# Performance work log

Measured on AMD Instinct MI355X. Metric: run time of the kernel, lower is better.

## Reference

```python
import jax, jax.numpy as jnp
import numpy as np

B, C, T = 1024, 64, 275
S = 10            # number of subjects
EMB = 184         # encoder embedding dim
PROJ = 1024       # projector dim
LN_EPS = 1e-5


def setup_inputs() -> dict:
    key = jax.random.key(0)
    ks = jax.random.split(key, 12)
    sc = lambda *shape: 1.0 / np.sqrt(shape[-1] if len(shape) > 1 else 1.0)
    return {
        "eeg": jax.random.normal(ks[0], (B, C, T), dtype=jnp.float32),
        "subject_ids": jax.random.randint(ks[1], (B,), 0, S, dtype=jnp.int64),
        # per-subject Linear(T, T): y = x @ W.T + b
        "subj_W": jax.random.normal(ks[2], (S, T, T), dtype=jnp.float32) / np.sqrt(T),
        "subj_b": jax.random.normal(ks[3], (S, T), dtype=jnp.float32) * 0.02,
        # encoder stub: flatten (C*T) -> Linear -> EMB
        "enc_W": jax.random.normal(ks[4], (C * T, EMB), dtype=jnp.float32) / np.sqrt(C * T),
        "enc_b": jnp.zeros((EMB,), dtype=jnp.float32),
        # projector: Linear(EMB, PROJ) -> ResidualAdd(GELU -> Linear(PROJ, PROJ)) -> LayerNorm
        "W1": jax.random.normal(ks[5], (EMB, PROJ), dtype=jnp.float32) / np.sqrt(EMB),
        "b1": jnp.zeros((PROJ,), dtype=jnp.float32),
        "W2": jax.random.normal(ks[6], (PROJ, PROJ), dtype=jnp.float32) / np.sqrt(PROJ),
        "b2": jnp.zeros((PROJ,), dtype=jnp.float32),
        "gamma": jnp.ones((PROJ,), dtype=jnp.float32),
        "beta": jnp.zeros((PROJ,), dtype=jnp.float32),
    }


def reference(eeg, subject_ids, subj_W, subj_b, enc_W, enc_b, W1, b1, W2, b2, gamma, beta):
    # --- subject-wise alignment: grouped gather -> linear -> scatter ---
    # Vectorized form of the per-subject loop: each row b uses weight subj_W[sid[b]].
    Wg = subj_W[subject_ids]              # [B, T, T]
    bg = subj_b[subject_ids]              # [B, T]
    # torch Linear: y = x @ W.T + b  ->  y[b,c,u] = sum_t eeg[b,c,t] * Wg[b,u,t]
    x = jnp.einsum("bct,but->bcu", eeg, Wg) + bg[:, None, :]   # [B, C, T]

    # --- encoder stub (SpatioTemporalCNN placeholder): flatten + linear ---
    h = x.reshape(x.shape[0], -1) @ enc_W + enc_b              # [B, EMB]

    # --- MLPProjector ---
    h = h @ W1 + b1                                            # [B, PROJ]
    r = jax.nn.gelu(h, approximate=False) @ W2 + b2            # dropout is identity at eval
    h = h + r
    # LayerNorm over last dim
    mu = jnp.mean(h, axis=-1, keepdims=True)
    var = jnp.mean(jnp.square(h - mu), axis=-1, keepdims=True)
    out = (h - mu) * jax.lax.rsqrt(var + LN_EPS) * gamma + beta
    return out
```

## Files before the change

### kernel.cpp

```cpp
#include <hip/hip_runtime.h>
#include <math.h>

#define B_N    1024
#define C_N    64
#define T_N    275
#define S_N    10
#define EMB_N  184
#define PROJ_N 1024
#define CT_N   (C_N * T_N)
#define TP     288
#define KP2    (TP * C_N)
#define EMBP   192
#define KZ2    32
#define KC2    (KP2 / KZ2)
#define KZ5    2
#define GMAX   264

typedef unsigned short u16;
typedef __attribute__((ext_vector_type(8))) short short8;
typedef __attribute__((ext_vector_type(4))) short short4v;
typedef __attribute__((ext_vector_type(4))) float f32x4;

#define MFMA16(a,b,c) __builtin_amdgcn_mfma_f32_16x16x32_bf16(a, b, c, 0, 0, 0)

__device__ __forceinline__ u16 f2bf(float f) {
    union { float f; unsigned u; } v; v.f = f;
    unsigned r = v.u + 0x7FFFu + ((v.u >> 16) & 1u);
    return (u16)(r >> 16);
}
__device__ __forceinline__ float gelu_exact(float v) {
    return 0.5f * v * (1.0f + erff(v * 0.70710678118654752f));
}
__device__ __forceinline__ void gload16(const void* g, void* lds) {
    __builtin_amdgcn_global_load_lds(
        (const __attribute__((address_space(1))) void*)g,
        (__attribute__((address_space(3))) void*)lds, 16, 0, 0);
}

__global__ __launch_bounds__(256) void p_all(
    const float* __restrict__ eeg, const int* __restrict__ sid,
    const float* __restrict__ W, const float* __restrict__ encW,
    const float* __restrict__ W1, const float* __restrict__ W2,
    u16* __restrict__ eegb, u16* __restrict__ Wb, u16* __restrict__ eT,
    u16* __restrict__ w1t, u16* __restrict__ w2t, int* __restrict__ bsq)
{
    __shared__ char smem[16640];
    const int blk = blockIdx.x;
    const int tid = threadIdx.x;

    if (blk < 1024) {
        const int b = blk;
        const float* src = eeg + (size_t)b * CT_N;
        u16* dst = eegb + (size_t)b * C_N * TP;
        #pragma unroll
        for (int p = 0; p < 9; ++p) {
            int ch = tid + p * 256;
            int c = ch / 36, q8 = ch - c * 36;
            int t0 = q8 * 8;
            short8 pk;
            #pragma unroll
            for (int e = 0; e < 8; ++e) {
                int t = t0 + e;
                float v = (t < T_N) ? src[c * T_N + t] : 0.f;
                pk[e] = (short)f2bf(v);
            }
            *reinterpret_cast<short8*>(dst + c * TP + t0) = pk;
        }
        return;
    }
    if (blk < 1834) {
        int idx4 = (blk - 1024) * 256 + tid;
        if (idx4 >= S_N * TP * TP / 4) return;
        int o = idx4 * 4;
        int row = o / TP, t = o - row * TP;
        int s = row / TP, u = row - s * TP;
        short4v pk;
        #pragma unroll
        for (int e = 0; e < 4; ++e) {
            float v = (u < T_N && t + e < T_N)
                ? W[((size_t)s * T_N + u) * T_N + t + e] : 0.f;
            pk[e] = (short)f2bf(v);
        }
        *reinterpret_cast<short4v*>(Wb + o) = pk;
        return;
    }
    if (blk < 2698) {
        float (*tile)[65] = (float(*)[65])smem;
        int local = blk - 1834;
        const int t = local / 3;
        const int n0 = (local % 3) * 64;
        const int j = tid & 63, cg = tid >> 6;
        #pragma unroll
        for (int pass = 0; pass < 16; ++pass) {
            int c = pass * 4 + cg;
            float v = 0.f;
            if (t < T_N && n0 + j < EMB_N)
                v = encW[((size_t)c * T_N + t) * EMB_N + n0 + j];
            tile[c][j] = v;
        }
        __syncthreads();
        #pragma unroll
        for (int pass = 0; pass < 16; ++pass) {
            int nl = pass * 4 + cg;
            eT[(size_t)(n0 + nl) * KP2 + t * 64 + j] = f2bf(tile[j][nl]);
        }
        return;
    }
    if (blk < 2746) {
        float (*tile)[65] = (float(*)[65])smem;
        int local = blk - 2698;
        const int k0 = (local % 3) * 64, n0 = (local / 3) * 64;
        for (int l = tid; l < 4096; l += 256) {
            int i = l >> 6, j = l & 63;
            float v = (k0 + i < EMB_N) ? W1[(size_t)(k0 + i) * PROJ_N + n0 + j] : 0.f;
            tile[i][j] = v;
        }
        __syncthreads();
        for (int l = tid; l < 4096; l += 256) {
            int j = l >> 6, i = l & 63;
            w1t[(size_t)(n0 + j) * EMBP + k0 + i] = f2bf(tile[i][j]);
        }
        return;
    }
    if (blk < 3002) {
        float (*tile)[65] = (float(*)[65])smem;
        int local = blk - 2746;
        const int k0 = (local % 16) * 64, n0 = (local / 16) * 64;
        for (int l = tid; l < 4096; l += 256) {
            int i = l >> 6, j = l & 63;
            tile[i][j] = W2[(size_t)(k0 + i) * PROJ_N + n0 + j];
        }
        __syncthreads();
        for (int l = tid; l < 4096; l += 256) {
            int j = l >> 6, i = l & 63;
            w2t[(size_t)(n0 + j) * PROJ_N + k0 + i] = f2bf(tile[i][j]);
        }
        return;
    }
    {
        int* sgrp = (int*)smem;
        int* C    = (int*)(smem + 4096);
        int* tot  = (int*)(smem + 4096 + 640);
        for (int i = tid; i < 1024; i += 256) sgrp[i] = sid[i];
        for (int i = tid; i < 4 * GMAX; i += 256) bsq[i] = -1;
        __syncthreads();
        const int w4 = tid >> 6, lane = tid & 63;
        #pragma unroll
        for (int j = 0; j < 4; ++j) {
            int chunk = w4 * 4 + j;
            int sb = sgrp[chunk * 64 + lane];
            int myc = 0;
            for (int s = 0; s < S_N; ++s) {
                unsigned long long m = __ballot(sb == s);
                if (lane == s) myc = (int)__popcll(m);
            }
            if (lane < S_N) C[chunk * S_N + lane] = myc;
        }
        __syncthreads();
        if (tid < S_N) {
            int a = 0;
            for (int w2 = 0; w2 < 16; ++w2) a += C[w2 * S_N + tid];
            tot[tid] = a;
        }
        __syncthreads();
        #pragma unroll
        for (int rep = 0; rep < 4; ++rep) {
            int b = tid + rep * 256;
            int s = sgrp[b];
            int off = 0;
            for (int s2 = 0; s2 < S_N; ++s2)
                if (s2 < s) off += (tot[s2] + 3) & ~3;
            int chunk = b >> 6;
            int rank = 0;
            for (int w2 = 0; w2 < 16; ++w2)
                if (w2 < chunk) rank += C[w2 * S_N + s];
            for (int i = chunk * 64; i < b; ++i) rank += (sgrp[i] == s) ? 1 : 0;
            bsq[off + rank] = b;
        }
    }
}

__global__ __launch_bounds__(512, 2) void k1g(
    const u16* __restrict__ eegb, const int* __restrict__ sid,
    const u16* __restrict__ Wb, const float* __restrict__ subj_b,
    const int* __restrict__ bsq, u16* __restrict__ xb)
{
    __shared__ u16 Bs[2][TP * 4 * 8];
    const int g = blockIdx.x;
    const int b0 = bsq[g * 4];
    if (b0 < 0) return;
    const int s = sid[b0];
    const int tid = threadIdx.x;
    const int w = tid >> 6, lane = tid & 63;
    const int bi = w >> 1, uh = w & 1;
    const int lrow = lane & 15, lk = lane >> 4;
    const int b = bsq[g * 4 + bi];
    const int bsafe = (b >= 0) ? b : 0;
    const u16* A = eegb + (size_t)bsafe * C_N * TP;
    const u16* Wr = Wb + (size_t)s * TP * TP;

    #define K1_STAGE(st, ks)                                                   \
        for (int l = tid; l < TP * 4; l += 512) {                              \
            int u_ = l >> 2, q_ = l & 3;                                       \
            gload16(Wr + (size_t)u_ * TP + (ks) * 32 + ((q_ ^ ((u_ >> 1) & 3)) << 3), \
                    &Bs[st][l * 8]);                                           \
        }

    f32x4 acc[4][9] = {};
    short8 a[4], an[4];

    K1_STAGE(0, 0);
    #pragma unroll
    for (int rt = 0; rt < 4; ++rt)
        a[rt] = *reinterpret_cast<const short8*>(A + (16 * rt + lrow) * TP + 8 * lk);
    __syncthreads();

    for (int ks = 0; ks < 9; ++ks) {
        const int st = ks & 1;
        if (ks < 8) {
            K1_STAGE(st ^ 1, ks + 1);
            #pragma unroll
            for (int rt = 0; rt < 4; ++rt)
                an[rt] = *reinterpret_cast<const short8*>(
                    A + (16 * rt + lrow) * TP + (ks + 1) * 32 + 8 * lk);
        }
        #pragma unroll
        for (int ct = 0; ct < 9; ++ct) {
            int u = uh * 144 + 16 * ct + lrow;
            int chunk = u * 4 + (lk ^ ((u >> 1) & 3));
            short8 bv = *reinterpret_cast<const short8*>(&Bs[st][chunk * 8]);
            #pragma unroll
            for (int rt = 0; rt < 4; ++rt)
                acc[rt][ct] = MFMA16(a[rt], bv, acc[rt][ct]);
        }
        __syncthreads();
        #pragma unroll
        for (int rt = 0; rt < 4; ++rt) a[rt] = an[rt];
    }

    if (b < 0) return;
    #pragma unroll
    for (int ct = 0; ct < 9; ++ct) {
        int u = uh * 144 + 16 * ct + lrow;
        if (u >= T_N) continue;
        float bias = subj_b[s * T_N + u];
        #pragma unroll
        for (int rt = 0; rt < 4; ++rt) {
            int c0 = 16 * rt + 4 * lk;
            short4v pk;
            #pragma unroll
            for (int r = 0; r < 4; ++r)
                pk[r] = (short)f2bf(acc[rt][ct][r] + bias);
            *reinterpret_cast<short4v*>(xb + ((size_t)b * TP + u) * C_N + c0) = pk;
        }
    }
    #undef K1_STAGE
}

__global__ __launch_bounds__(256) void k2_mfma(
    const u16* __restrict__ xb, const u16* __restrict__ eT,
    float* __restrict__ part)
{
    __shared__ u16 Ab[2][128 * 64];
    const int m0 = blockIdx.x * 128;
    const int kz = blockIdx.y;
    const int kbase = kz * KC2;
    const int tid = threadIdx.x;
    const int w = tid >> 6, lane = tid & 63;
    const int lrow = lane & 15, lk = lane >> 4;

    #define K2_STAGE(st, step)                                                 \
        _Pragma("unroll")                                                      \
        for (int p = 0; p < 4; ++p) {                                          \
            int l = tid + p * 256;                                             \
            int r_ = l >> 3, q_ = l & 7;                                       \
            gload16(xb + (size_t)(m0 + r_) * KP2 + kbase + (step) * 64 +       \
                        ((q_ ^ (r_ & 7)) << 3),                                \
                    &Ab[st][l * 8]);                                           \
        }

    #define K2_BLOAD(step, dst)                                                \
        _Pragma("unroll")                                                      \
        for (int ct = 0; ct < 3; ++ct)                                         \
            _Pragma("unroll")                                                  \
            for (int ki = 0; ki < 2; ++ki)                                     \
                dst[ct][ki] = *reinterpret_cast<const short8*>(                \
                    eT + (size_t)(48 * w + 16 * ct + lrow) * KP2 + kbase +     \
                    (step) * 64 + ki * 32 + 8 * lk);

    f32x4 acc[8][3] = {};
    short8 bf[3][2], bn[3][2];

    K2_STAGE(0, 0);
    K2_BLOAD(0, bf);
    __syncthreads();

    for (int step = 0; step < 9; ++step) {
        const int st = step & 1;
        if (step < 8) {
            K2_STAGE(st ^ 1, step + 1);
            K2_BLOAD(step + 1, bn);
        }
        #pragma unroll
        for (int ki = 0; ki < 2; ++ki)
            #pragma unroll
            for (int rt = 0; rt < 8; ++rt) {
                int m = 16 * rt + lrow;
                int chunk = m * 8 + ((4 * ki + lk) ^ (m & 7));
                short8 af = *reinterpret_cast<const short8*>(&Ab[st][chunk * 8]);
                #pragma unroll
                for (int ct = 0; ct < 3; ++ct)
                    acc[rt][ct] = MFMA16(af, bf[ct][ki], acc[rt][ct]);
            }
        __syncthreads();
        #pragma unroll
        for (int ct = 0; ct < 3; ++ct)
            #pragma unroll
            for (int ki = 0; ki < 2; ++ki) bf[ct][ki] = bn[ct][ki];
    }

    #pragma unroll
    for (int rt = 0; rt < 8; ++rt)
        #pragma unroll
        for (int ct = 0; ct < 3; ++ct) {
            int n = 48 * w + 16 * ct + lrow;
            #pragma unroll
            for (int r = 0; r < 4; ++r) {
                int m = m0 + 16 * rt + 4 * lk + r;
                part[((size_t)kz * B_N + m) * EMBP + n] = acc[rt][ct][r];
            }
        }
    #undef K2_STAGE
    #undef K2_BLOAD
}

__global__ __launch_bounds__(256) void k3_reduce(
    const float* __restrict__ part, const float* __restrict__ enc_b,
    u16* __restrict__ hb)
{
    int idx = blockIdx.x * 256 + threadIdx.x;
    if (idx >= B_N * EMBP) return;
    int n = idx % EMBP;
    float s = 0.f;
    if (n < EMB_N) {
        s = enc_b[n];
        #pragma unroll
        for (int z = 0; z < KZ2; ++z)
            s += part[(size_t)z * B_N * EMBP + idx];
    }
    hb[idx] = f2bf(s);
}

__global__ __launch_bounds__(256) void k4_mfma(
    const u16* __restrict__ hb, const u16* __restrict__ w1t,
    const float* __restrict__ b1, float* __restrict__ h1, u16* __restrict__ g)
{
    __shared__ u16 Ab[64 * EMBP];
    __shared__ u16 Bb[64 * EMBP];
    const int m0 = blockIdx.x * 64, n0 = blockIdx.y * 64;
    const int tid = threadIdx.x;
    const int w = tid >> 6, lane = tid & 63;
    const int wr = w >> 1, wc = w & 1;
    const int lrow = lane & 15, lk = lane >> 4;

    #pragma unroll
    for (int i = 0; i < 6; ++i) {
        int L = tid + i * 256;
        int row = L / 24, qp = L % 24;
        int ql = qp ^ (row & 7);
        gload16(hb  + (size_t)(m0 + row) * EMBP + ql * 8, &Ab[(size_t)L * 8]);
        gload16(w1t + (size_t)(n0 + row) * EMBP + ql * 8, &Bb[(size_t)L * 8]);
    }
    __syncthreads();

    f32x4 acc[2][2] = {};
    #pragma unroll
    for (int ks = 0; ks < 6; ++ks) {
        #pragma unroll
        for (int rt = 0; rt < 2; ++rt) {
            int c = 32 * wr + 16 * rt + lrow;
            short8 af = *reinterpret_cast<const short8*>(
                &Ab[c * EMBP + (((4 * ks + lk) ^ (c & 7)) * 8)]);
            #pragma unroll
            for (int ct = 0; ct < 2; ++ct) {
                int nl = 32 * wc + 16 * ct + lrow;
                short8 bfv = *reinterpret_cast<const short8*>(
                    &Bb[nl * EMBP + (((4 * ks + lk) ^ (nl & 7)) * 8)]);
                acc[rt][ct] = MFMA16(af, bfv, acc[rt][ct]);
            }
        }
    }
    #pragma unroll
    for (int rt = 0; rt < 2; ++rt)
        #pragma unroll
        for (int ct = 0; ct < 2; ++ct) {
            int n = n0 + 32 * wc + 16 * ct + lrow;
            #pragma unroll
            for (int r = 0; r < 4; ++r) {
                int m = m0 + 32 * wr + 16 * rt + 4 * lk + r;
                float v = acc[rt][ct][r] + b1[n];
                size_t o = (size_t)m * PROJ_N + n;
                h1[o] = v;
                g[o] = f2bf(gelu_exact(v));
            }
        }
}

__global__ __launch_bounds__(256) void k5_mfma(
    const u16* __restrict__ g, const u16* __restrict__ w2t,
    float* __restrict__ part2)
{
    __shared__ u16 Ab[2][64 * 64];
    __shared__ u16 Bb[2][64 * 64];
    const int m0 = blockIdx.x * 64, n0 = blockIdx.y * 64;
    const int kz = blockIdx.z;
    const int kbase = kz * (PROJ_N / KZ5);
    const int tid = threadIdx.x;
    const int w = tid >> 6, lane = tid & 63;
    const int wr = w >> 1, wc = w & 1;
    const int lrow = lane & 15, lk = lane >> 4;

    const int r0 = tid >> 3, q0 = tid & 7;
    const int r1 = (tid + 256) >> 3;
    const u16* a0 = g + (size_t)(m0 + r0) * PROJ_N + (q0 ^ (r0 & 7)) * 8;
    const u16* a1 = g + (size_t)(m0 + r1) * PROJ_N + (q0 ^ (r1 & 7)) * 8;
    const u16* b0 = w2t + (size_t)(n0 + r0) * PROJ_N + (q0 ^ (r0 & 7)) * 8;
    const u16* b1p = w2t + (size_t)(n0 + r1) * PROJ_N + (q0 ^ (r1 & 7)) * 8;

    f32x4 acc[2][2] = {};
    int buf = 0;
    gload16(a0 + kbase, &Ab[0][(size_t)(w * 64) * 8]);
    gload16(a1 + kbase, &Ab[0][(size_t)(w * 64 + 256) * 8]);
    gload16(b0 + kbase, &Bb[0][(size_t)(w * 64) * 8]);
    gload16(b1p + kbase, &Bb[0][(size_t)(w * 64 + 256) * 8]);
    __syncthreads();

    for (int step = 0; step < 8; ++step) {
        if (step < 7) {
            int k0 = kbase + (step + 1) * 64;
            gload16(a0 + k0, &Ab[buf ^ 1][(size_t)(w * 64) * 8]);
            gload16(a1 + k0, &Ab[buf ^ 1][(size_t)(w * 64 + 256) * 8]);
            gload16(b0 + k0, &Bb[buf ^ 1][(size_t)(w * 64) * 8]);
            gload16(b1p + k0, &Bb[buf ^ 1][(size_t)(w * 64 + 256) * 8]);
        }
        #pragma unroll
        for (int ki = 0; ki < 2; ++ki) {
            #pragma unroll
            for (int rt = 0; rt < 2; ++rt) {
                int c = 32 * wr + 16 * rt + lrow;
                short8 af = *reinterpret_cast<const short8*>(
                    &Ab[buf][c * 64 + (((lk + 4 * ki) ^ (c & 7)) * 8)]);
                #pragma unroll
                for (int ct = 0; ct < 2; ++ct) {
                    int nl = 32 * wc + 16 * ct + lrow;
                    short8 bfv = *reinterpret_cast<const short8*>(
                        &Bb[buf][nl * 64 + (((lk + 4 * ki) ^ (nl & 7)) * 8)]);
                    acc[rt][ct] = MFMA16(af, bfv, acc[rt][ct]);
                }
            }
        }
        __syncthreads();
        buf ^= 1;
    }
    #pragma unroll
    for (int rt = 0; rt < 2; ++rt)
        #pragma unroll
        for (int ct = 0; ct < 2; ++ct) {
            int n = n0 + 32 * wc + 16 * ct + lrow;
            #pragma unroll
            for (int r = 0; r < 4; ++r) {
                int m = m0 + 32 * wr + 16 * rt + 4 * lk + r;
                part2[(size_t)kz * B_N * PROJ_N + (size_t)m * PROJ_N + n] = acc[rt][ct][r];
            }
        }
}

__global__ __launch_bounds__(256) void k5r_ln(
    const float* __restrict__ part2, const float* __restrict__ h1,
    const float* __restrict__ b2, const float* __restrict__ gamma,
    const float* __restrict__ beta, float* __restrict__ out)
{
    const int m = blockIdx.x;
    const int tid = threadIdx.x;
    const float4* h4 = reinterpret_cast<const float4*>(h1 + (size_t)m * PROJ_N);
    const float4* p0 = reinterpret_cast<const float4*>(part2 + (size_t)m * PROJ_N);
    const float4* p1 = reinterpret_cast<const float4*>(part2 + (size_t)(B_N + m) * PROJ_N);
    const float4* b4 = reinterpret_cast<const float4*>(b2);
    float4 va = h4[tid], vb = p0[tid], vc = p1[tid], vd = b4[tid];
    float v[4] = { va.x + vb.x + vc.x + vd.x, va.y + vb.y + vc.y + vd.y,
                   va.z + vb.z + vc.z + vd.z, va.w + vb.w + vc.w + vd.w };
    float s = 0.f, sq = 0.f;
    #pragma unroll
    for (int i = 0; i < 4; ++i) { s += v[i]; sq += v[i] * v[i]; }
    #pragma unroll
    for (int off = 32; off > 0; off >>= 1) {
        s  += __shfl_down(s, off);
        sq += __shfl_down(sq, off);
    }
    __shared__ float ss[4], ssq[4];
    int wid = tid >> 6, lane = tid & 63;
    if (lane == 0) { ss[wid] = s; ssq[wid] = sq; }
    __syncthreads();
    if (tid == 0) {
        float a = 0.f, bsum = 0.f;
        #pragma unroll
        for (int q = 0; q < 4; ++q) { a += ss[q]; bsum += ssq[q]; }
        ss[0] = a; ssq[0] = bsum;
    }
    __syncthreads();
    float mu  = ss[0] * (1.0f / PROJ_N);
    float var = ssq[0] * (1.0f / PROJ_N) - mu * mu;
    float rs  = rsqrtf(var + 1e-5f);
    const float4 g4 = reinterpret_cast<const float4*>(gamma)[tid];
    const float4 be4 = reinterpret_cast<const float4*>(beta)[tid];
    float gg[4] = { g4.x, g4.y, g4.z, g4.w };
    float bb[4] = { be4.x, be4.y, be4.z, be4.w };
    float4 o4;
    float* op = reinterpret_cast<float*>(&o4);
    #pragma unroll
    for (int i = 0; i < 4; ++i) op[i] = (v[i] - mu) * rs * gg[i] + bb[i];
    reinterpret_cast<float4*>(out + (size_t)m * PROJ_N)[tid] = o4;
}

extern "C" void kernel_launch(void* const* d_in, const int* in_sizes, int n_in,
                              void* d_out, int out_size, void* d_ws, size_t ws_size,
                              hipStream_t stream)
{
    const float* eeg    = (const float*)d_in[0];
    const int*   sid    = (const int*)  d_in[1];
    const float* subj_W = (const float*)d_in[2];
    const float* subj_b = (const float*)d_in[3];
    const float* enc_W  = (const float*)d_in[4];
    const float* enc_b  = (const float*)d_in[5];
    const float* W1     = (const float*)d_in[6];
    const float* b1     = (const float*)d_in[7];
    const float* W2     = (const float*)d_in[8];
    const float* b2     = (const float*)d_in[9];
    const float* gamma  = (const float*)d_in[10];
    const float* beta   = (const float*)d_in[11];
    float* out = (float*)d_out;

    char* w = (char*)d_ws;
    u16*   xb    = (u16*)(w);
    u16*   Wb    = (u16*)(w + 37748736);
    u16*   eT    = (u16*)(w + 39407616);
    u16*   w1t   = (u16*)(w + 46485504);
    u16*   w2t   = (u16*)(w + 46878720);
    u16*   hb    = (u16*)(w + 48975872);
    float* h1    = (float*)(w + 49369088);
    u16*   g     = (u16*)(w + 53563392);
    int*   bsq   = (int*)(w + 55660544);
    char*  scr   = w + 55664896;
    u16*   eegb  = (u16*)scr;
    float* part  = (float*)scr;
    float* part2 = (float*)(scr + 25165824);

    p_all<<<dim3(3003), 256, 0, stream>>>(eeg, sid, subj_W, enc_W, W1, W2,
                                          eegb, Wb, eT, w1t, w2t, bsq);
    k1g  <<<dim3(GMAX), 512, 0, stream>>>(eegb, sid, Wb, subj_b, bsq, xb);
    k2_mfma<<<dim3(8, KZ2), 256, 0, stream>>>(xb, eT, part);
    k3_reduce<<<dim3((B_N * EMBP + 255) / 256), 256, 0, stream>>>(part, enc_b, hb);
    k4_mfma<<<dim3(16, 16), 256, 0, stream>>>(hb, w1t, b1, h1, g);
    k5_mfma<<<dim3(16, 16, KZ5), 256, 0, stream>>>(g, w2t, part2);
    k5r_ln <<<dim3(B_N), 256, 0, stream>>>(part2, h1, b2, gamma, beta, out);
}
```

Before: 132.2 us.

## Fuse eeg bf16 conversion into grouped subject GEMM and retile encoder GEMM

Drops the separate eeg-to-bf16 pre-pass: k1g now reads fp32 eeg directly, converts it in registers and stages it through double-buffered LDS, with the MFMA operands swapped so the output is written in channel-major [c][u] layout. The encoder weight transpose and the k2 K-ordering change to match this layout, and subject bias is pre-padded into a small buffer. k2 moves to 64-row tiles with half the split-K factor, giving more M blocks and fewer partials to reduce. This removes a full write and re-read of the bf16 eeg copy, at the cost of more complex staging and register pressure in k1g.

Result: slower. 173.6 us (+31.4%).

```diff
diff --git a/kernel.cpp b/kernel.cpp
--- a/kernel.cpp
+++ b/kernel.cpp
@@ -9,12 +9,19 @@
 #define PROJ_N 1024
 #define CT_N   (C_N * T_N)
 #define TP     288
-#define KP2    (TP * C_N)
+#define KP2    (C_N * TP)
 #define EMBP   192
-#define KZ2    32
+#define KZ2    16
 #define KC2    (KP2 / KZ2)
 #define KZ5    2
 #define GMAX   264
+
+#define SEC_W   0
+#define SEC_E   810
+#define SEC_1   1002
+#define SEC_2   1050
+#define SEC_G   1306
+#define SEC_N   1307
 
 typedef unsigned short u16;
 typedef __attribute__((ext_vector_type(8))) short short8;
@@ -38,38 +45,18 @@
 }
 
 __global__ __launch_bounds__(256) void p_all(
-    const float* __restrict__ eeg, const int* __restrict__ sid,
-    const float* __restrict__ W, const float* __restrict__ encW,
-    const float* __restrict__ W1, const float* __restrict__ W2,
-    u16* __restrict__ eegb, u16* __restrict__ Wb, u16* __restrict__ eT,
-    u16* __restrict__ w1t, u16* __restrict__ w2t, int* __restrict__ bsq)
+    const int* __restrict__ sid, const float* __restrict__ W,
+    const float* __restrict__ encW, const float* __restrict__ W1,
+    const float* __restrict__ W2, const float* __restrict__ subj_b,
+    u16* __restrict__ Wb, u16* __restrict__ eT, u16* __restrict__ w1t,
+    u16* __restrict__ w2t, int* __restrict__ bsq, float* __restrict__ sbp)
 {
     __shared__ char smem[16640];
     const int blk = blockIdx.x;
     const int tid = threadIdx.x;
 
-    if (blk < 1024) {
-        const int b = blk;
-        const float* src = eeg + (size_t)b * CT_N;
-        u16* dst = eegb + (size_t)b * C_N * TP;
-        #pragma unroll
-        for (int p = 0; p < 9; ++p) {
-            int ch = tid + p * 256;
-            int c = ch / 36, q8 = ch - c * 36;
-            int t0 = q8 * 8;
-            short8 pk;
-            #pragma unroll
-            for (int e = 0; e < 8; ++e) {
-                int t = t0 + e;
-                float v = (t < T_N) ? src[c * T_N + t] : 0.f;
-                pk[e] = (short)f2bf(v);
-            }
-            *reinterpret_cast<short8*>(dst + c * TP + t0) = pk;
-        }
-        return;
-    }
-    if (blk < 1834) {
-        int idx4 = (blk - 1024) * 256 + tid;
+    if (blk < SEC_E) {
+        int idx4 = blk * 256 + tid;
         if (idx4 >= S_N * TP * TP / 4) return;
         int o = idx4 * 4;
         int row = o / TP, t = o - row * TP;
@@ -84,31 +71,35 @@
         *reinterpret_cast<short4v*>(Wb + o) = pk;
         return;
     }
-    if (blk < 2698) {
+    if (blk < SEC_1) {
         float (*tile)[65] = (float(*)[65])smem;
-        int local = blk - 1834;
-        const int t = local / 3;
+        int local = blk - SEC_E;
+        const int c = local / 3;
         const int n0 = (local % 3) * 64;
-        const int j = tid & 63, cg = tid >> 6;
-        #pragma unroll
-        for (int pass = 0; pass < 16; ++pass) {
-            int c = pass * 4 + cg;
-            float v = 0.f;
-            if (t < T_N && n0 + j < EMB_N)
-                v = encW[((size_t)c * T_N + t) * EMB_N + n0 + j];
-            tile[c][j] = v;
-        }
-        __syncthreads();
-        #pragma unroll
-        for (int pass = 0; pass < 16; ++pass) {
-            int nl = pass * 4 + cg;
-            eT[(size_t)(n0 + nl) * KP2 + t * 64 + j] = f2bf(tile[j][nl]);
+        for (int u0 = 0; u0 < TP; u0 += 64) {
+            int wlen = (TP - u0 < 64) ? (TP - u0) : 64;
+            __syncthreads();
+            for (int l = tid; l < 4096; l += 256) {
+                int i = l >> 6, j = l & 63;
+                int u = u0 + i, n = n0 + j;
+                float v = 0.f;
+                if (u < T_N && n < EMB_N)
+                    v = encW[((size_t)c * T_N + u) * EMB_N + n];
+                tile[i][j] = v;
+            }
+            __syncthreads();
+            for (int l = tid; l < 4096; l += 256) {
+                int j = l >> 6, i = l & 63;
+                if (i < wlen)
+                    eT[(size_t)(n0 + j) * KP2 + (size_t)c * TP + u0 + i] =
+                        f2bf(tile[i][j]);
+            }
         }
         return;
     }
-    if (blk < 2746) {
+    if (blk < SEC_2) {
         float (*tile)[65] = (float(*)[65])smem;
-        int local = blk - 2698;
+        int local = blk - SEC_1;
         const int k0 = (local % 3) * 64, n0 = (local / 3) * 64;
         for (int l = tid; l < 4096; l += 256) {
             int i = l >> 6, j = l & 63;
@@ -122,9 +113,9 @@
         }
         return;
     }
-    if (blk < 3002) {
+    if (blk < SEC_G) {
         float (*tile)[65] = (float(*)[65])smem;
-        int local = blk - 2746;
+        int local = blk - SEC_2;
         const int k0 = (local % 16) * 64, n0 = (local / 16) * 64;
         for (int l = tid; l < 4096; l += 256) {
             int i = l >> 6, j = l & 63;
@@ -138,6 +129,10 @@
         return;
     }
     {
+        for (int i = tid; i < S_N * TP; i += 256) {
+            int s = i / TP, u = i - s * TP;
+            sbp[i] = (u < T_N) ? subj_b[s * T_N + u] : 0.f;
+        }
         int* sgrp = (int*)smem;
         int* C    = (int*)(smem + 4096);
         int* tot  = (int*)(smem + 4096 + 640);
@@ -181,11 +176,12 @@
 }
 
 __global__ __launch_bounds__(512, 2) void k1g(
-    const u16* __restrict__ eegb, const int* __restrict__ sid,
-    const u16* __restrict__ Wb, const float* __restrict__ subj_b,
+    const float* __restrict__ eeg, const int* __restrict__ sid,
+    const u16* __restrict__ Wb, const float* __restrict__ sbp,
     const int* __restrict__ bsq, u16* __restrict__ xb)
 {
-    __shared__ u16 Bs[2][TP * 4 * 8];
+    __shared__ __align__(16) u16 Ws[2][TP * 32];
+    __shared__ __align__(16) u16 Es[2][256 * 40];
     const int g = blockIdx.x;
     const int b0 = bsq[g * 4];
     if (b0 < 0) return;
@@ -195,74 +191,97 @@
     const int bi = w >> 1, uh = w & 1;
     const int lrow = lane & 15, lk = lane >> 4;
     const int b = bsq[g * 4 + bi];
-    const int bsafe = (b >= 0) ? b : 0;
-    const u16* A = eegb + (size_t)bsafe * C_N * TP;
     const u16* Wr = Wb + (size_t)s * TP * TP;
 
-    #define K1_STAGE(st, ks)                                                   \
+    const int srow = tid >> 1;
+    const int bt = srow >> 6, ct = srow & 63;
+    const int half = tid & 1;
+    int bstage = bsq[g * 4 + bt]; if (bstage < 0) bstage = b0;
+    const float* esrc = eeg + (size_t)bstage * CT_N + ct * T_N;
+
+    #define K1_WSTAGE(st, ks)                                                  \
         for (int l = tid; l < TP * 4; l += 512) {                              \
             int u_ = l >> 2, q_ = l & 3;                                       \
             gload16(Wr + (size_t)u_ * TP + (ks) * 32 + ((q_ ^ ((u_ >> 1) & 3)) << 3), \
-                    &Bs[st][l * 8]);                                           \
-        }
-
-    f32x4 acc[4][9] = {};
-    short8 a[4], an[4];
-
-    K1_STAGE(0, 0);
-    #pragma unroll
-    for (int rt = 0; rt < 4; ++rt)
-        a[rt] = *reinterpret_cast<const short8*>(A + (16 * rt + lrow) * TP + 8 * lk);
+                    &Ws[st][l * 8]);                                           \
+        }
+    #define K1_ELOAD(ks, v)                                                    \
+        _Pragma("unroll")                                                      \
+        for (int e = 0; e < 16; ++e) {                                         \
+            int t_ = (ks) * 32 + half * 16 + e;                                \
+            v[e] = (t_ < T_N) ? esrc[t_] : 0.f;                                \
+        }
+    #define K1_EWRITE(st, v)                                                   \
+        {   short8 p0_, p1_;                                                   \
+            _Pragma("unroll")                                                  \
+            for (int e = 0; e < 8; ++e) p0_[e] = (short)f2bf(v[e]);            \
+            _Pragma("unroll")                                                  \
+            for (int e = 0; e < 8; ++e) p1_[e] = (short)f2bf(v[e + 8]);        \
+            *reinterpret_cast<short8*>(&Es[st][srow * 40 + half * 16]) = p0_;  \
+            *reinterpret_cast<short8*>(&Es[st][srow * 40 + half * 16 + 8]) = p1_; \
+        }
+
+    f32x4 acc[9][4] = {};
+    float ev[16], evn[16];
+
+    K1_WSTAGE(0, 0);
+    K1_ELOAD(0, ev);
+    K1_EWRITE(0, ev);
     __syncthreads();
 
     for (int ks = 0; ks < 9; ++ks) {
         const int st = ks & 1;
         if (ks < 8) {
-            K1_STAGE(st ^ 1, ks + 1);
-            #pragma unroll
-            for (int rt = 0; rt < 4; ++rt)
-                an[rt] = *reinterpret_cast<const short8*>(
-                    A + (16 * rt + lrow) * TP + (ks + 1) * 32 + 8 * lk);
-        }
-        #pragma unroll
-        for (int ct = 0; ct < 9; ++ct) {
-            int u = uh * 144 + 16 * ct + lrow;
+            K1_WSTAGE(st ^ 1, ks + 1);
+            K1_ELOAD(ks + 1, evn);
+        }
+        short8 ef[4];
+        #pragma unroll
+        for (int cf = 0; cf < 4; ++cf)
+            ef[cf] = *reinterpret_cast<const short8*>(
+                &Es[st][(bi * 64 + cf * 16 + lrow) * 40 + lk * 8]);
+        #pragma unroll
+        for (int uf = 0; uf < 9; ++uf) {
+            int u = uh * 144 + uf * 16 + lrow;
             int chunk = u * 4 + (lk ^ ((u >> 1) & 3));
-            short8 bv = *reinterpret_cast<const short8*>(&Bs[st][chunk * 8]);
-            #pragma unroll
-            for (int rt = 0; rt < 4; ++rt)
-                acc[rt][ct] = MFMA16(a[rt], bv, acc[rt][ct]);
-        }
-        __syncthreads();
-        #pragma unroll
-        for (int rt = 0; rt < 4; ++rt) a[rt] = an[rt];
+            short8 av = *reinterpret_cast<const short8*>(&Ws[st][chunk * 8]);
+            #pragma unroll
+            for (int cf = 0; cf < 4; ++cf)
+                acc[uf][cf] = MFMA16(av, ef[cf], acc[uf][cf]);
+        }
+        if (ks < 8) K1_EWRITE(st ^ 1, evn);
+        __syncthreads();
     }
 
     if (b < 0) return;
-    #pragma unroll
-    for (int ct = 0; ct < 9; ++ct) {
-        int u = uh * 144 + 16 * ct + lrow;
-        if (u >= T_N) continue;
-        float bias = subj_b[s * T_N + u];
-        #pragma unroll
-        for (int rt = 0; rt < 4; ++rt) {
-            int c0 = 16 * rt + 4 * lk;
+    u16* xrow = xb + (size_t)b * KP2;
+    #pragma unroll
+    for (int uf = 0; uf < 9; ++uf) {
+        int ub = uh * 144 + uf * 16 + 4 * lk;
+        float4 b4 = *reinterpret_cast<const float4*>(sbp + s * TP + ub);
+        float bias[4] = { b4.x, b4.y, b4.z, b4.w };
+        #pragma unroll
+        for (int cf = 0; cf < 4; ++cf) {
+            int c = cf * 16 + lrow;
             short4v pk;
             #pragma unroll
             for (int r = 0; r < 4; ++r)
-                pk[r] = (short)f2bf(acc[rt][ct][r] + bias);
-            *reinterpret_cast<short4v*>(xb + ((size_t)b * TP + u) * C_N + c0) = pk;
-        }
-    }
-    #undef K1_STAGE
+                pk[r] = (ub + r < T_N) ? (short)f2bf(acc[uf][cf][r] + bias[r])
+                                       : (short)0;
+            *reinterpret_cast<short4v*>(xrow + (size_t)c * TP + ub) = pk;
+        }
+    }
+    #undef K1_WSTAGE
+    #undef K1_ELOAD
+    #undef K1_EWRITE
 }
 
 __global__ __launch_bounds__(256) void k2_mfma(
     const u16* __restrict__ xb, const u16* __restrict__ eT,
     float* __restrict__ part)
 {
-    __shared__ u16 Ab[2][128 * 64];
-    const int m0 = blockIdx.x * 128;
+    __shared__ __align__(16) u16 Ab[2][64 * 64];
+    const int m0 = blockIdx.x * 64;
     const int kz = blockIdx.y;
     const int kbase = kz * KC2;
     const int tid = threadIdx.x;
@@ -271,14 +290,13 @@
 
     #define K2_STAGE(st, step)                                                 \
         _Pragma("unroll")                                                      \
-        for (int p = 0; p < 4; ++p) {                                          \
+        for (int p = 0; p < 2; ++p) {                                          \
             int l = tid + p * 256;                                             \
             int r_ = l >> 3, q_ = l & 7;                                       \
             gload16(xb + (size_t)(m0 + r_) * KP2 + kbase + (step) * 64 +       \
                         ((q_ ^ (r_ & 7)) << 3),                                \
                     &Ab[st][l * 8]);                                           \
         }
-
     #define K2_BLOAD(step, dst)                                                \
         _Pragma("unroll")                                                      \
         for (int ct = 0; ct < 3; ++ct)                                         \
@@ -288,23 +306,23 @@
                     eT + (size_t)(48 * w + 16 * ct + lrow) * KP2 + kbase +     \
                     (step) * 64 + ki * 32 + 8 * lk);
 
-    f32x4 acc[8][3] = {};
+    f32x4 acc[4][3] = {};
     short8 bf[3][2], bn[3][2];
 
     K2_STAGE(0, 0);
     K2_BLOAD(0, bf);
     __syncthreads();
 
-    for (int step = 0; step < 9; ++step) {
+    for (int step = 0; step < 18; ++step) {
         const int st = step & 1;
-        if (step < 8) {
+        if (step < 17) {
             K2_STAGE(st ^ 1, step + 1);
             K2_BLOAD(step + 1, bn);
         }
         #pragma unroll
         for (int ki = 0; ki < 2; ++ki)
             #pragma unroll
-            for (int rt = 0; rt < 8; ++rt) {
+            for (int rt = 0; rt < 4; ++rt) {
                 int m = 16 * rt + lrow;
                 int chunk = m * 8 + ((4 * ki + lk) ^ (m & 7));
                 short8 af = *reinterpret_cast<const short8*>(&Ab[st][chunk * 8]);
@@ -320,7 +338,7 @@
     }
 
     #pragma unroll
-    for (int rt = 0; rt < 8; ++rt)
+    for (int rt = 0; rt < 4; ++rt)
         #pragma unroll
         for (int ct = 0; ct < 3; ++ct) {
             int n = 48 * w + 16 * ct + lrow;
@@ -355,8 +373,8 @@
     const u16* __restrict__ hb, const u16* __restrict__ w1t,
     const float* __restrict__ b1, float* __restrict__ h1, u16* __restrict__ g)
 {
-    __shared__ u16 Ab[64 * EMBP];
-    __shared__ u16 Bb[64 * EMBP];
+    __shared__ __align__(16) u16 Ab[64 * EMBP];
+    __shared__ __align__(16) u16 Bb[64 * EMBP];
     const int m0 = blockIdx.x * 64, n0 = blockIdx.y * 64;
     const int tid = threadIdx.x;
     const int w = tid >> 6, lane = tid & 63;
@@ -410,8 +428,8 @@
     const u16* __restrict__ g, const u16* __restrict__ w2t,
     float* __restrict__ part2)
 {
-    __shared__ u16 Ab[2][64 * 64];
-    __shared__ u16 Bb[2][64 * 64];
+    __shared__ __align__(16) u16 Ab[2][64 * 64];
+    __shared__ __align__(16) u16 Bb[2][64 * 64];
     const int m0 = blockIdx.x * 64, n0 = blockIdx.y * 64;
     const int kz = blockIdx.z;
     const int kbase = kz * (PROJ_N / KZ5);
@@ -549,16 +567,15 @@
     u16*   hb    = (u16*)(w + 48975872);
     float* h1    = (float*)(w + 49369088);
     u16*   g     = (u16*)(w + 53563392);
-    int*   bsq   = (int*)(w + 55660544);
-    char*  scr   = w + 55664896;
-    u16*   eegb  = (u16*)scr;
-    float* part  = (float*)scr;
-    float* part2 = (float*)(scr + 25165824);
-
-    p_all<<<dim3(3003), 256, 0, stream>>>(eeg, sid, subj_W, enc_W, W1, W2,
-                                          eegb, Wb, eT, w1t, w2t, bsq);
-    k1g  <<<dim3(GMAX), 512, 0, stream>>>(eegb, sid, Wb, subj_b, bsq, xb);
-    k2_mfma<<<dim3(8, KZ2), 256, 0, stream>>>(xb, eT, part);
+    float* sbp   = (float*)(w + 55660544);
+    int*   bsq   = (int*)(w + 55672064);
+    float* part  = (float*)(w + 55676288);
+    float* part2 = (float*)(w + 68259200);
+
+    p_all<<<dim3(SEC_N), 256, 0, stream>>>(sid, subj_W, enc_W, W1, W2, subj_b,
+                                           Wb, eT, w1t, w2t, bsq, sbp);
+    k1g  <<<dim3(GMAX), 512, 0, stream>>>(eeg, sid, Wb, sbp, bsq, xb);
+    k2_mfma<<<dim3(16, KZ2), 256, 0, stream>>>(xb, eT, part);
     k3_reduce<<<dim3((B_N * EMBP + 255) / 256), 256, 0, stream>>>(part, enc_b, hb);
     k4_mfma<<<dim3(16, 16), 256, 0, stream>>>(hb, w1t, b1, h1, g);
     k5_mfma<<<dim3(16, 16, KZ5), 256, 0, stream>>>(g, w2t, part2);
```
